# Kernel tuning notes

Measured on AMD Instinct MI355X. Metric: run time of the kernel, lower is better.

## Reference

```python
import jax, jax.numpy as jnp
import numpy as np

SMOOTH = 1.0
IGNORE_INDEX = 255


def setup_inputs() -> dict:
    key = jax.random.key(0)
    k1, k2 = jax.random.split(key)
    B, C, H, W = 8, 19, 512, 512
    logits = jax.random.normal(k1, (B, C, H, W), dtype=jnp.float32)
    targets = jax.random.randint(k2, (B, H, W), 0, C, dtype=jnp.int64)
    return {"logits": logits, "targets": targets}


def reference(logits, targets):
    B, C, H, W = logits.shape
    probs = jax.nn.softmax(logits, axis=1)                      # [B,C,H,W]
    valid = targets != IGNORE_INDEX                             # [B,H,W] bool
    vf = valid.astype(probs.dtype)                              # [B,H,W]
    # clamp invalid labels to 0; their contributions are zeroed by vf
    t = jnp.where(valid, targets, 0).reshape(-1)                # [B*H*W]
    # per-class sum of probs over valid pixels (replaces boolean compaction)
    probs_sum = jnp.einsum('bchw,bhw->c', probs, vf)            # [C]
    # prob assigned to the true class at each pixel (replaces one-hot * probs)
    gathered = jnp.take_along_axis(probs, jnp.where(valid, targets, 0)[:, None], axis=1)[:, 0]  # [B,H,W]
    gathered = (gathered * vf).reshape(-1)
    intersection = jnp.zeros((C,), probs.dtype).at[t].add(gathered)   # [C]
    counts = jnp.zeros((C,), probs.dtype).at[t].add(vf.reshape(-1))   # [C] = one_hot.sum(0)
    union = probs_sum + counts
    dice = (2.0 * intersection + SMOOTH) / (union + SMOOTH)
    loss = (1.0 - dice).mean()
    # torch returns logits.sum()*0 when no valid pixels
    return jnp.where(vf.sum() > 0, loss, logits.sum() * 0.0)
```

## Files before the change

kernel.cpp:

```cpp
#include <hip/hip_runtime.h>
#include <hip/hip_bf16.h>
#include <math.h>


#define CC 19
#define HWBITS 18
#define HHWW (1 << HWBITS)
#define NPIX (8 * HHWW)
#define QPP (HHWW / 4)
#define NQUAD (NPIX / 4)
#define NBLK 1024
#define NTHR 256
#define NTH_TOT (NBLK * NTHR)
#define NITER (NQUAD / NTH_TOT)
#define IGNORE_IDX 255

typedef float f32x4 __attribute__((ext_vector_type(4)));
typedef int   i32x4 __attribute__((ext_vector_type(4)));

__global__ __launch_bounds__(NTHR, 2) void dice_accum(
    const float* __restrict__ logits,
    const int* __restrict__ targets,
    float* __restrict__ part)
{
    const int tid = blockIdx.x * NTHR + threadIdx.x;

    float accS[CC], accI[CC], accC[CC];
#pragma unroll
    for (int c = 0; c < CC; ++c) { accS[c] = 0.f; accI[c] = 0.f; accC[c] = 0.f; }

#pragma unroll 1
    for (int it = 0; it < NITER; ++it) {
        const int q = tid + it * NTH_TOT;
        const int b = q >> 16;
        const int hw4 = q & (QPP - 1);
        const f32x4* base = (const f32x4*)logits + (size_t)(b * CC) * QPP + hw4;

        f32x4 x[CC];
#pragma unroll
        for (int c = 0; c < CC; ++c)
            x[c] = __builtin_nontemporal_load(base + (size_t)c * QPP);
        const i32x4 tt = __builtin_nontemporal_load(
            (const i32x4*)(targets + 4 * (size_t)q));

        float s0 = 0.f, s1 = 0.f, s2 = 0.f, s3 = 0.f;
#pragma unroll
        for (int c = 0; c < CC; ++c) {
            x[c].x = __expf(x[c].x); s0 += x[c].x;
            x[c].y = __expf(x[c].y); s1 += x[c].y;
            x[c].z = __expf(x[c].z); s2 += x[c].z;
            x[c].w = __expf(x[c].w); s3 += x[c].w;
        }
        const float i0 = (tt.x != IGNORE_IDX) ? __builtin_amdgcn_rcpf(s0) : 0.f;
        const float i1 = (tt.y != IGNORE_IDX) ? __builtin_amdgcn_rcpf(s1) : 0.f;
        const float i2 = (tt.z != IGNORE_IDX) ? __builtin_amdgcn_rcpf(s2) : 0.f;
        const float i3 = (tt.w != IGNORE_IDX) ? __builtin_amdgcn_rcpf(s3) : 0.f;

#pragma unroll
        for (int c = 0; c < CC; ++c) {
            accS[c] = fmaf(x[c].x, i0,
                      fmaf(x[c].y, i1,
                      fmaf(x[c].z, i2,
                      fmaf(x[c].w, i3, accS[c]))));
            const bool h0 = (tt.x == c), h1 = (tt.y == c);
            const bool h2 = (tt.z == c), h3 = (tt.w == c);
            accI[c] = fmaf(h0 ? x[c].x : 0.f, i0,
                      fmaf(h1 ? x[c].y : 0.f, i1,
                      fmaf(h2 ? x[c].z : 0.f, i2,
                      fmaf(h3 ? x[c].w : 0.f, i3, accI[c]))));
            accC[c] += (h0 ? 1.f : 0.f) + (h1 ? 1.f : 0.f)
                     + (h2 ? 1.f : 0.f) + (h3 ? 1.f : 0.f);
        }
    }

#pragma unroll
    for (int c = 0; c < CC; ++c) {
        for (int off = 32; off; off >>= 1) {
            accS[c] += __shfl_down(accS[c], off);
            accI[c] += __shfl_down(accI[c], off);
            accC[c] += __shfl_down(accC[c], off);
        }
    }

    __shared__ float s_part[4][64];
    const int wave = threadIdx.x >> 6;
    const int lane = threadIdx.x & 63;
    if (lane == 0) {
#pragma unroll
        for (int c = 0; c < CC; ++c) {
            s_part[wave][c]          = accS[c];
            s_part[wave][CC + c]     = accI[c];
            s_part[wave][2 * CC + c] = accC[c];
        }
#pragma unroll
        for (int c = 3 * CC; c < 64; ++c) s_part[wave][c] = 0.f;
    }
    __syncthreads();
    if (threadIdx.x < 64) {
        float v = s_part[0][threadIdx.x] + s_part[1][threadIdx.x]
                + s_part[2][threadIdx.x] + s_part[3][threadIdx.x];
        part[blockIdx.x * 64 + threadIdx.x] = v;
    }
}

__global__ __launch_bounds__(1024) void dice_final(
    const float* __restrict__ part, float* __restrict__ out)
{
    const int wave = threadIdx.x >> 6;
    const int lane = threadIdx.x & 63;
    float v = 0.f;
    for (int r = wave; r < NBLK; r += 16)
        v += part[r * 64 + lane];

    __shared__ float s_red[16][64];
    s_red[wave][lane] = v;
    __syncthreads();

    __shared__ float s_tot[64];
    if (threadIdx.x < 64) {
        float tot = 0.f;
#pragma unroll
        for (int w = 0; w < 16; ++w) tot += s_red[w][threadIdx.x];
        s_tot[threadIdx.x] = tot;
    }
    __syncthreads();

    if (threadIdx.x == 0) {
        float loss = 0.f, totv = 0.f;
#pragma unroll
        for (int c = 0; c < CC; ++c) {
            const float S = s_tot[c];
            const float I = s_tot[CC + c];
            const float N = s_tot[2 * CC + c];
            totv += N;
            loss += 1.f - (2.f * I + 1.f) / (S + N + 1.f);
        }
        out[0] = (totv > 0.f) ? loss * (1.f / (float)CC) : 0.f;
    }
}

extern "C" void kernel_launch(void* const* d_in, const int* in_sizes, int n_in,
                              void* d_out, int out_size, void* d_ws, size_t ws_size,
                              hipStream_t stream) {
    const float* logits = (const float*)d_in[0];
    const int* targets = (const int*)d_in[1];
    float* part = (float*)d_ws;
    float* out = (float*)d_out;

    dice_accum<<<NBLK, NTHR, 0, stream>>>(logits, targets, part);
    dice_final<<<1, 1024, 0, stream>>>(part, out);
}
```

Measured before the change: 229.4 us.

## Two-pass softmax per thread: reload logits instead of holding them in registers

Each thread now handles four quads in one shot (no loop). A first pass sums the exponentials across classes. A second pass reloads the logits, recomputes the exponentials and accumulates the per-class statistics, so the 19 loaded vectors no longer have to stay live in registers. This lowers register pressure and exposes more independent loads per thread. The cost is reading the logits twice (the second read may hit in cache) and computing every exp twice. The grid is halved to 512 blocks, and the nontemporal loads are dropped.

```diff
diff --git a/kernel.cpp b/kernel.cpp
--- a/kernel.cpp
+++ b/kernel.cpp
@@ -1,76 +1,116 @@
 #include <hip/hip_runtime.h>
-#include <hip/hip_bf16.h>
 #include <math.h>
 
 
 #define CC 19
-#define HWBITS 18
-#define HHWW (1 << HWBITS)
-#define NPIX (8 * HHWW)
-#define QPP (HHWW / 4)
-#define NQUAD (NPIX / 4)
-#define NBLK 1024
+#define QPP 65536
+#define NQUAD 524288
+#define NBLK 512
 #define NTHR 256
-#define NTH_TOT (NBLK * NTHR)
-#define NITER (NQUAD / NTH_TOT)
+#define QPB 1024
 #define IGNORE_IDX 255
 
 typedef float f32x4 __attribute__((ext_vector_type(4)));
 typedef int   i32x4 __attribute__((ext_vector_type(4)));
+
+__device__ __forceinline__ f32x4 exp4(f32x4 v) {
+    f32x4 r;
+    r.x = __expf(v.x); r.y = __expf(v.y);
+    r.z = __expf(v.z); r.w = __expf(v.w);
+    return r;
+}
 
 __global__ __launch_bounds__(NTHR, 2) void dice_accum(
     const float* __restrict__ logits,
     const int* __restrict__ targets,
     float* __restrict__ part)
 {
-    const int tid = blockIdx.x * NTHR + threadIdx.x;
+    const int lane = threadIdx.x & 63;
+    const int wv   = threadIdx.x >> 6;
+    const int q0   = blockIdx.x * QPB + wv * 256 + lane;
+    const int b    = q0 >> 16;
+    const int hw4  = q0 & (QPP - 1);
+    const f32x4* bbase = (const f32x4*)logits + (size_t)b * (CC * QPP) + hw4;
+
+    const i32x4* tq = (const i32x4*)targets;
+    const i32x4 t0 = tq[q0];
+    const i32x4 t1 = tq[q0 + 64];
+    const i32x4 t2 = tq[q0 + 128];
+    const i32x4 t3 = tq[q0 + 192];
+
+    f32x4 s0 = {0.f,0.f,0.f,0.f}, s1 = {0.f,0.f,0.f,0.f};
+    f32x4 s2 = {0.f,0.f,0.f,0.f}, s3 = {0.f,0.f,0.f,0.f};
+#pragma unroll
+    for (int c = 0; c < CC; ++c) {
+        const f32x4* p = bbase + (size_t)c * QPP;
+        s0 += exp4(p[0]);
+        s1 += exp4(p[64]);
+        s2 += exp4(p[128]);
+        s3 += exp4(p[192]);
+    }
+
+    f32x4 i0, i1, i2, i3;
+    i0.x = (t0.x != IGNORE_IDX) ? __builtin_amdgcn_rcpf(s0.x) : 0.f;
+    i0.y = (t0.y != IGNORE_IDX) ? __builtin_amdgcn_rcpf(s0.y) : 0.f;
+    i0.z = (t0.z != IGNORE_IDX) ? __builtin_amdgcn_rcpf(s0.z) : 0.f;
+    i0.w = (t0.w != IGNORE_IDX) ? __builtin_amdgcn_rcpf(s0.w) : 0.f;
+    i1.x = (t1.x != IGNORE_IDX) ? __builtin_amdgcn_rcpf(s1.x) : 0.f;
+    i1.y = (t1.y != IGNORE_IDX) ? __builtin_amdgcn_rcpf(s1.y) : 0.f;
+    i1.z = (t1.z != IGNORE_IDX) ? __builtin_amdgcn_rcpf(s1.z) : 0.f;
+    i1.w = (t1.w != IGNORE_IDX) ? __builtin_amdgcn_rcpf(s1.w) : 0.f;
+    i2.x = (t2.x != IGNORE_IDX) ? __builtin_amdgcn_rcpf(s2.x) : 0.f;
+    i2.y = (t2.y != IGNORE_IDX) ? __builtin_amdgcn_rcpf(s2.y) : 0.f;
+    i2.z = (t2.z != IGNORE_IDX) ? __builtin_amdgcn_rcpf(s2.z) : 0.f;
+    i2.w = (t2.w != IGNORE_IDX) ? __builtin_amdgcn_rcpf(s2.w) : 0.f;
+    i3.x = (t3.x != IGNORE_IDX) ? __builtin_amdgcn_rcpf(s3.x) : 0.f;
+    i3.y = (t3.y != IGNORE_IDX) ? __builtin_amdgcn_rcpf(s3.y) : 0.f;
+    i3.z = (t3.z != IGNORE_IDX) ? __builtin_amdgcn_rcpf(s3.z) : 0.f;
+    i3.w = (t3.w != IGNORE_IDX) ? __builtin_amdgcn_rcpf(s3.w) : 0.f;
 
     float accS[CC], accI[CC], accC[CC];
 #pragma unroll
     for (int c = 0; c < CC; ++c) { accS[c] = 0.f; accI[c] = 0.f; accC[c] = 0.f; }
 
-#pragma unroll 1
-    for (int it = 0; it < NITER; ++it) {
-        const int q = tid + it * NTH_TOT;
-        const int b = q >> 16;
-        const int hw4 = q & (QPP - 1);
-        const f32x4* base = (const f32x4*)logits + (size_t)(b * CC) * QPP + hw4;
+#pragma unroll
+    for (int c = 0; c < CC; ++c) {
+        const f32x4* p = bbase + (size_t)c * QPP;
+        const f32x4 eA = exp4(p[0]);
+        const f32x4 eB = exp4(p[64]);
+        const f32x4 eC = exp4(p[128]);
+        const f32x4 eD = exp4(p[192]);
 
-        f32x4 x[CC];
-#pragma unroll
-        for (int c = 0; c < CC; ++c)
-            x[c] = __builtin_nontemporal_load(base + (size_t)c * QPP);
-        const i32x4 tt = __builtin_nontemporal_load(
-            (const i32x4*)(targets + 4 * (size_t)q));
+        accS[c] = fmaf(eA.x, i0.x, fmaf(eA.y, i0.y, fmaf(eA.z, i0.z, fmaf(eA.w, i0.w,
+                  fmaf(eB.x, i1.x, fmaf(eB.y, i1.y, fmaf(eB.z, i1.z, fmaf(eB.w, i1.w,
+                  fmaf(eC.x, i2.x, fmaf(eC.y, i2.y, fmaf(eC.z, i2.z, fmaf(eC.w, i2.w,
+                  fmaf(eD.x, i3.x, fmaf(eD.y, i3.y, fmaf(eD.z, i3.z, fmaf(eD.w, i3.w,
+                  accS[c]))))))))))))))));
 
-        float s0 = 0.f, s1 = 0.f, s2 = 0.f, s3 = 0.f;
-#pragma unroll
-        for (int c = 0; c < CC; ++c) {
-            x[c].x = __expf(x[c].x); s0 += x[c].x;
-            x[c].y = __expf(x[c].y); s1 += x[c].y;
-            x[c].z = __expf(x[c].z); s2 += x[c].z;
-            x[c].w = __expf(x[c].w); s3 += x[c].w;
-        }
-        const float i0 = (tt.x != IGNORE_IDX) ? __builtin_amdgcn_rcpf(s0) : 0.f;
-        const float i1 = (tt.y != IGNORE_IDX) ? __builtin_amdgcn_rcpf(s1) : 0.f;
-        const float i2 = (tt.z != IGNORE_IDX) ? __builtin_amdgcn_rcpf(s2) : 0.f;
-        const float i3 = (tt.w != IGNORE_IDX) ? __builtin_amdgcn_rcpf(s3) : 0.f;
+        accI[c] = fmaf((t0.x == c) ? eA.x : 0.f, i0.x,
+                  fmaf((t0.y == c) ? eA.y : 0.f, i0.y,
+                  fmaf((t0.z == c) ? eA.z : 0.f, i0.z,
+                  fmaf((t0.w == c) ? eA.w : 0.f, i0.w,
+                  fmaf((t1.x == c) ? eB.x : 0.f, i1.x,
+                  fmaf((t1.y == c) ? eB.y : 0.f, i1.y,
+                  fmaf((t1.z == c) ? eB.z : 0.f, i1.z,
+                  fmaf((t1.w == c) ? eB.w : 0.f, i1.w,
+                  fmaf((t2.x == c) ? eC.x : 0.f, i2.x,
+                  fmaf((t2.y == c) ? eC.y : 0.f, i2.y,
+                  fmaf((t2.z == c) ? eC.z : 0.f, i2.z,
+                  fmaf((t2.w == c) ? eC.w : 0.f, i2.w,
+                  fmaf((t3.x == c) ? eD.x : 0.f, i3.x,
+                  fmaf((t3.y == c) ? eD.y : 0.f, i3.y,
+                  fmaf((t3.z == c) ? eD.z : 0.f, i3.z,
+                  fmaf((t3.w == c) ? eD.w : 0.f, i3.w,
+                  accI[c]))))))))))))))));
 
-#pragma unroll
-        for (int c = 0; c < CC; ++c) {
-            accS[c] = fmaf(x[c].x, i0,
-                      fmaf(x[c].y, i1,
-                      fmaf(x[c].z, i2,
-                      fmaf(x[c].w, i3, accS[c]))));
-            const bool h0 = (tt.x == c), h1 = (tt.y == c);
-            const bool h2 = (tt.z == c), h3 = (tt.w == c);
-            accI[c] = fmaf(h0 ? x[c].x : 0.f, i0,
-                      fmaf(h1 ? x[c].y : 0.f, i1,
-                      fmaf(h2 ? x[c].z : 0.f, i2,
-                      fmaf(h3 ? x[c].w : 0.f, i3, accI[c]))));
-            accC[c] += (h0 ? 1.f : 0.f) + (h1 ? 1.f : 0.f)
-                     + (h2 ? 1.f : 0.f) + (h3 ? 1.f : 0.f);
-        }
+        accC[c] += ((t0.x == c) ? 1.f : 0.f) + ((t0.y == c) ? 1.f : 0.f)
+                 + ((t0.z == c) ? 1.f : 0.f) + ((t0.w == c) ? 1.f : 0.f)
+                 + ((t1.x == c) ? 1.f : 0.f) + ((t1.y == c) ? 1.f : 0.f)
+                 + ((t1.z == c) ? 1.f : 0.f) + ((t1.w == c) ? 1.f : 0.f)
+                 + ((t2.x == c) ? 1.f : 0.f) + ((t2.y == c) ? 1.f : 0.f)
+                 + ((t2.z == c) ? 1.f : 0.f) + ((t2.w == c) ? 1.f : 0.f)
+                 + ((t3.x == c) ? 1.f : 0.f) + ((t3.y == c) ? 1.f : 0.f)
+                 + ((t3.z == c) ? 1.f : 0.f) + ((t3.w == c) ? 1.f : 0.f);
     }
 
 #pragma unroll
@@ -83,17 +123,15 @@
     }
 
     __shared__ float s_part[4][64];
-    const int wave = threadIdx.x >> 6;
-    const int lane = threadIdx.x & 63;
     if (lane == 0) {
 #pragma unroll
         for (int c = 0; c < CC; ++c) {
-            s_part[wave][c]          = accS[c];
-            s_part[wave][CC + c]     = accI[c];
-            s_part[wave][2 * CC + c] = accC[c];
+            s_part[wv][c]          = accS[c];
+            s_part[wv][CC + c]     = accI[c];
+            s_part[wv][2 * CC + c] = accC[c];
         }
 #pragma unroll
-        for (int c = 3 * CC; c < 64; ++c) s_part[wave][c] = 0.f;
+        for (int c = 3 * CC; c < 64; ++c) s_part[wv][c] = 0.f;
     }
     __syncthreads();
     if (threadIdx.x < 64) {
```

Measured after the change: 297.4 us. 1.3x slower.

## Double-buffer float2 tile loads and reduce partials with global atomics

Applied to the files above, without the earlier changes.

The main loop now works on float2 tiles with two register buffers. The next tile's loads are issued before the current tile is processed, with sched_barrier keeping the compiler from reordering them, so memory latency overlaps the exp and accumulate work. The per-block partial array is replaced by atomicAdd into 57 global sums zeroed by a memset, and the final kernel shrinks to a single wave. This adds a memset launch and atomic contention on 57 addresses, and float atomics make the summation order nondeterministic.

```diff
diff --git a/kernel.cpp b/kernel.cpp
--- a/kernel.cpp
+++ b/kernel.cpp
@@ -1,27 +1,58 @@
 #include <hip/hip_runtime.h>
-#include <hip/hip_bf16.h>
 #include <math.h>
 
 
 #define CC 19
-#define HWBITS 18
-#define HHWW (1 << HWBITS)
-#define NPIX (8 * HHWW)
-#define QPP (HHWW / 4)
-#define NQUAD (NPIX / 4)
+#define HPP 131072
 #define NBLK 1024
 #define NTHR 256
 #define NTH_TOT (NBLK * NTHR)
-#define NITER (NQUAD / NTH_TOT)
+#define NITER 4
 #define IGNORE_IDX 255
 
-typedef float f32x4 __attribute__((ext_vector_type(4)));
-typedef int   i32x4 __attribute__((ext_vector_type(4)));
+typedef float f32x2 __attribute__((ext_vector_type(2)));
+typedef int   i32x2 __attribute__((ext_vector_type(2)));
+
+__device__ __forceinline__ void issue_tile(
+    f32x2 (&x)[CC], i32x2& t,
+    const float* __restrict__ logits, const int* __restrict__ targets, int hq)
+{
+    const int b   = hq >> 17;
+    const int hw2 = hq & (HPP - 1);
+    const f32x2* base = (const f32x2*)logits + ((size_t)b * CC) * HPP + hw2;
+#pragma unroll
+    for (int c = 0; c < CC; ++c)
+        x[c] = __builtin_nontemporal_load(base + (size_t)c * HPP);
+    t = __builtin_nontemporal_load((const i32x2*)targets + hq);
+    __builtin_amdgcn_sched_barrier(0);
+}
+
+__device__ __forceinline__ void proc_tile(
+    f32x2 (&x)[CC], const i32x2 t,
+    float (&accS)[CC], float (&accI)[CC], float (&accC)[CC])
+{
+    float s0 = 0.f, s1 = 0.f;
+#pragma unroll
+    for (int c = 0; c < CC; ++c) {
+        x[c].x = __expf(x[c].x); s0 += x[c].x;
+        x[c].y = __expf(x[c].y); s1 += x[c].y;
+    }
+    const float i0 = (t.x != IGNORE_IDX) ? __builtin_amdgcn_rcpf(s0) : 0.f;
+    const float i1 = (t.y != IGNORE_IDX) ? __builtin_amdgcn_rcpf(s1) : 0.f;
+#pragma unroll
+    for (int c = 0; c < CC; ++c) {
+        accS[c] = fmaf(x[c].x, i0, fmaf(x[c].y, i1, accS[c]));
+        const bool h0 = (t.x == c), h1 = (t.y == c);
+        accI[c] = fmaf(h0 ? x[c].x : 0.f, i0,
+                  fmaf(h1 ? x[c].y : 0.f, i1, accI[c]));
+        accC[c] += (h0 ? 1.f : 0.f) + (h1 ? 1.f : 0.f);
+    }
+}
 
 __global__ __launch_bounds__(NTHR, 2) void dice_accum(
     const float* __restrict__ logits,
     const int* __restrict__ targets,
-    float* __restrict__ part)
+    float* __restrict__ sums)
 {
     const int tid = blockIdx.x * NTHR + threadIdx.x;
 
@@ -29,49 +60,17 @@
 #pragma unroll
     for (int c = 0; c < CC; ++c) { accS[c] = 0.f; accI[c] = 0.f; accC[c] = 0.f; }
 
-#pragma unroll 1
-    for (int it = 0; it < NITER; ++it) {
-        const int q = tid + it * NTH_TOT;
-        const int b = q >> 16;
-        const int hw4 = q & (QPP - 1);
-        const f32x4* base = (const f32x4*)logits + (size_t)(b * CC) * QPP + hw4;
+    f32x2 xa[CC], xb[CC];
+    i32x2 t0, t1, t2, t3;
 
-        f32x4 x[CC];
-#pragma unroll
-        for (int c = 0; c < CC; ++c)
-            x[c] = __builtin_nontemporal_load(base + (size_t)c * QPP);
-        const i32x4 tt = __builtin_nontemporal_load(
-            (const i32x4*)(targets + 4 * (size_t)q));
-
-        float s0 = 0.f, s1 = 0.f, s2 = 0.f, s3 = 0.f;
-#pragma unroll
-        for (int c = 0; c < CC; ++c) {
-            x[c].x = __expf(x[c].x); s0 += x[c].x;
-            x[c].y = __expf(x[c].y); s1 += x[c].y;
-            x[c].z = __expf(x[c].z); s2 += x[c].z;
-            x[c].w = __expf(x[c].w); s3 += x[c].w;
-        }
-        const float i0 = (tt.x != IGNORE_IDX) ? __builtin_amdgcn_rcpf(s0) : 0.f;
-        const float i1 = (tt.y != IGNORE_IDX) ? __builtin_amdgcn_rcpf(s1) : 0.f;
-        const float i2 = (tt.z != IGNORE_IDX) ? __builtin_amdgcn_rcpf(s2) : 0.f;
-        const float i3 = (tt.w != IGNORE_IDX) ? __builtin_amdgcn_rcpf(s3) : 0.f;
-
-#pragma unroll
-        for (int c = 0; c < CC; ++c) {
-            accS[c] = fmaf(x[c].x, i0,
-                      fmaf(x[c].y, i1,
-                      fmaf(x[c].z, i2,
-                      fmaf(x[c].w, i3, accS[c]))));
-            const bool h0 = (tt.x == c), h1 = (tt.y == c);
-            const bool h2 = (tt.z == c), h3 = (tt.w == c);
-            accI[c] = fmaf(h0 ? x[c].x : 0.f, i0,
-                      fmaf(h1 ? x[c].y : 0.f, i1,
-                      fmaf(h2 ? x[c].z : 0.f, i2,
-                      fmaf(h3 ? x[c].w : 0.f, i3, accI[c]))));
-            accC[c] += (h0 ? 1.f : 0.f) + (h1 ? 1.f : 0.f)
-                     + (h2 ? 1.f : 0.f) + (h3 ? 1.f : 0.f);
-        }
-    }
+    issue_tile(xa, t0, logits, targets, tid);
+    issue_tile(xb, t1, logits, targets, tid + NTH_TOT);
+    proc_tile(xa, t0, accS, accI, accC);
+    issue_tile(xa, t2, logits, targets, tid + 2 * NTH_TOT);
+    proc_tile(xb, t1, accS, accI, accC);
+    issue_tile(xb, t3, logits, targets, tid + 3 * NTH_TOT);
+    proc_tile(xa, t2, accS, accI, accC);
+    proc_tile(xb, t3, accS, accI, accC);
 
 #pragma unroll
     for (int c = 0; c < CC; ++c) {
@@ -92,51 +91,34 @@
             s_part[wave][CC + c]     = accI[c];
             s_part[wave][2 * CC + c] = accC[c];
         }
-#pragma unroll
-        for (int c = 3 * CC; c < 64; ++c) s_part[wave][c] = 0.f;
     }
     __syncthreads();
-    if (threadIdx.x < 64) {
-        float v = s_part[0][threadIdx.x] + s_part[1][threadIdx.x]
-                + s_part[2][threadIdx.x] + s_part[3][threadIdx.x];
-        part[blockIdx.x * 64 + threadIdx.x] = v;
+    if (threadIdx.x < 3 * CC) {
+        const float v = s_part[0][threadIdx.x] + s_part[1][threadIdx.x]
+                      + s_part[2][threadIdx.x] + s_part[3][threadIdx.x];
+        atomicAdd(&sums[threadIdx.x], v);
     }
 }
 
-__global__ __launch_bounds__(1024) void dice_final(
-    const float* __restrict__ part, float* __restrict__ out)
+__global__ __launch_bounds__(64) void dice_final(
+    const float* __restrict__ sums, float* __restrict__ out)
 {
-    const int wave = threadIdx.x >> 6;
-    const int lane = threadIdx.x & 63;
-    float v = 0.f;
-    for (int r = wave; r < NBLK; r += 16)
-        v += part[r * 64 + lane];
-
-    __shared__ float s_red[16][64];
-    s_red[wave][lane] = v;
-    __syncthreads();
-
-    __shared__ float s_tot[64];
-    if (threadIdx.x < 64) {
-        float tot = 0.f;
+    const int c = threadIdx.x;
+    float term = 0.f, tv = 0.f;
+    if (c < CC) {
+        const float S = sums[c];
+        const float I = sums[CC + c];
+        const float N = sums[2 * CC + c];
+        tv = N;
+        term = 1.f - (2.f * I + 1.f) / (S + N + 1.f);
+    }
 #pragma unroll
-        for (int w = 0; w < 16; ++w) tot += s_red[w][threadIdx.x];
-        s_tot[threadIdx.x] = tot;
+    for (int off = 32; off; off >>= 1) {
+        term += __shfl_down(term, off);
+        tv   += __shfl_down(tv, off);
     }
-    __syncthreads();
-
-    if (threadIdx.x == 0) {
-        float loss = 0.f, totv = 0.f;
-#pragma unroll
-        for (int c = 0; c < CC; ++c) {
-            const float S = s_tot[c];
-            const float I = s_tot[CC + c];
-            const float N = s_tot[2 * CC + c];
-            totv += N;
-            loss += 1.f - (2.f * I + 1.f) / (S + N + 1.f);
-        }
-        out[0] = (totv > 0.f) ? loss * (1.f / (float)CC) : 0.f;
-    }
+    if (c == 0)
+        out[0] = (tv > 0.f) ? term * (1.f / (float)CC) : 0.f;
 }
 
 extern "C" void kernel_launch(void* const* d_in, const int* in_sizes, int n_in,
@@ -144,9 +126,10 @@
                               hipStream_t stream) {
     const float* logits = (const float*)d_in[0];
     const int* targets = (const int*)d_in[1];
-    float* part = (float*)d_ws;
+    float* sums = (float*)d_ws;
     float* out = (float*)d_out;
 
-    dice_accum<<<NBLK, NTHR, 0, stream>>>(logits, targets, part);
-    dice_final<<<1, 1024, 0, stream>>>(part, out);
+    hipMemsetAsync(sums, 0, 64 * sizeof(float), stream);
+    dice_accum<<<NBLK, NTHR, 0, stream>>>(logits, targets, sums);
+    dice_final<<<1, 64, 0, stream>>>(sums, out);
 }
```

Result: no change. 229.4 us (-0.0%).
